# Kernel optimization log

Hardware: AMD Instinct MI355X
Metric: run time of the kernel (lower is better)

Reference implementation:

```python
import jax, jax.numpy as jnp
import numpy as np

B, S, E = 8, 2048, 1024
DROPOUT_P = 0.1


def setup_inputs() -> dict:
    key = jax.random.key(0)
    kq, kk, kv, km, kw, kb = jax.random.split(key, 6)
    query = jax.random.normal(kq, (B, S, E), dtype=jnp.float32)
    key_t = jax.random.normal(kk, (B, S, E), dtype=jnp.float32)
    value = jax.random.normal(kv, (B, S, E), dtype=jnp.float32)
    # inverted dropout mask: keep with prob 1-p, scale kept by 1/(1-p)
    keep = jax.random.bernoulli(km, 1.0 - DROPOUT_P, (B, S, S))
    dropout_mask = keep.astype(jnp.float32) / (1.0 - DROPOUT_P)
    Wout = jax.random.normal(kw, (E, E), dtype=jnp.float32) * (E ** -0.5)
    bout = jax.random.normal(kb, (E,), dtype=jnp.float32) * 0.01
    return {
        "query": query,
        "key": key_t,
        "value": value,
        "dropout_mask": dropout_mask,
        "Wout": Wout,
        "bout": bout,
        "inv_scale_factor": 32,  # sqrt(E) = sqrt(1024)
    }


def reference(query, key, value, dropout_mask, Wout, bout, inv_scale_factor):
    # scores: [B, S, S]
    scores = jnp.einsum("bqd,bkd->bqk", query, key) / jnp.float32(inv_scale_factor)
    probs = jax.nn.softmax(scores, axis=-1)
    probs = probs * dropout_mask  # inverted dropout
    attn = jnp.einsum("bqk,bkd->bqd", probs, value)  # [B, S, E]
    # fc_out: torch Linear -> x @ W.T + b
    return jnp.einsum("bqd,ed->bqe", attn, Wout) + bout
```

## Files before the change

kernel.cpp:

```cpp
#include <hip/hip_runtime.h>
#include <cstdint>
#include <cstddef>

typedef short short8 __attribute__((ext_vector_type(8)));
typedef float f32x4 __attribute__((ext_vector_type(4)));

static __device__ __forceinline__ ushort f2bf(float f) {
  union { float f; uint32_t u; } v; v.f = f;
  uint32_t u = v.u + 0x7fffu + ((v.u >> 16) & 1u);
  return (ushort)(u >> 16);
}
static __device__ __forceinline__ float b2f(uint32_t u) {
  union { uint32_t u; float f; } v; v.u = u << 16;
  return v.f;
}

static __device__ __forceinline__ void g2lds16(const ushort* g, ushort* lds) {
  __builtin_amdgcn_global_load_lds(
      (const __attribute__((address_space(1))) void*)(uintptr_t)g,
      (__attribute__((address_space(3))) void*)(uintptr_t)lds,
      16, 0, 0);
}

__global__ __launch_bounds__(256) void convert_qk_bf16(
    const float* __restrict__ Q, const float* __restrict__ K,
    ushort* __restrict__ Qb, ushort* __restrict__ Kb) {
  const bool second = blockIdx.x >= 8192;
  const float* src = second ? K : Q;
  ushort* dst = second ? Kb : Qb;
  const size_t i = ((size_t)(blockIdx.x & 8191) * 256 + threadIdx.x) * 8;
  const float4 a = *(const float4*)(src + i);
  const float4 b = *(const float4*)(src + i + 4);
  ushort4 o0, o1;
  o0.x = f2bf(a.x); o0.y = f2bf(a.y); o0.z = f2bf(a.z); o0.w = f2bf(a.w);
  o1.x = f2bf(b.x); o1.y = f2bf(b.y); o1.z = f2bf(b.z); o1.w = f2bf(b.w);
  *(ushort4*)(dst + i) = o0;
  *(ushort4*)(dst + i + 4) = o1;
}

__global__ __launch_bounds__(256) void transpose_convert_v(
    const float* __restrict__ V, ushort* __restrict__ Vt) {
  __shared__ float t[32][33];
  const int b = blockIdx.z;
  const int d0 = blockIdx.x * 32;
  const int k0 = blockIdx.y * 32;
  const int tx = threadIdx.x, ty = threadIdx.y;
  const float* Vb = V + (size_t)b * 2048 * 1024;
  ushort* Vtb = Vt + (size_t)b * 1024 * 2048;
#pragma unroll
  for (int j = 0; j < 32; j += 8)
    t[ty + j][tx] = Vb[(size_t)(k0 + ty + j) * 1024 + d0 + tx];
  __syncthreads();
  const int l = ty * 32 + tx;
  const int kk = (l & 15) * 2;
  const int dd = l >> 4;
#pragma unroll
  for (int p = 0; p < 2; ++p) {
    const int d = dd + p * 16;
    const uint32_t val =
        (uint32_t)f2bf(t[kk][d]) | ((uint32_t)f2bf(t[kk + 1][d]) << 16);
    *(uint32_t*)&Vtb[(size_t)(d0 + d) * 2048 + k0 + kk] = val;
  }
}

template <bool B_F32, bool OUT_BF16, bool BIAS>
__global__ __launch_bounds__(256) void gemm_bt(
    const ushort* __restrict__ Ap, const void* __restrict__ Bp,
    void* __restrict__ Cp, int M, int N, int K,
    size_t sA, size_t sB, size_t sC, float scale,
    const float* __restrict__ bias) {
  constexpr int BK = 64;
  constexpr int LDB = B_F32 ? 72 : 64;
  __shared__ __align__(16) ushort As[128 * 64];
  __shared__ __align__(16) ushort Bs[128 * LDB];
  const int tid = threadIdx.x;
  const int z = blockIdx.z;
  const int bm = blockIdx.y, bn = blockIdx.x;
  const int lane = tid & 63, w = tid >> 6;
  const int quad = lane >> 4, l16 = lane & 15;
  const int row0 = (w & 1) * 64, col0 = (w >> 1) * 64;
  const int srow = lane >> 3;
  const int scol = ((lane & 7) ^ srow) * 8;

  f32x4 acc[4][4];
#pragma unroll
  for (int i = 0; i < 4; ++i)
#pragma unroll
    for (int j = 0; j < 4; ++j) acc[i][j] = (f32x4){0.f, 0.f, 0.f, 0.f};

  const ushort* Abase = Ap + sA * z + (size_t)bm * 128 * K;

  for (int k0 = 0; k0 < K; k0 += BK) {
#pragma unroll
    for (int i = 0; i < 4; ++i) {
      const int rbase = w * 8 + i * 32;
      g2lds16(Abase + (size_t)(rbase + srow) * K + k0 + scol, &As[rbase * 64]);
    }
    if constexpr (B_F32) {
      const float* B = (const float*)Bp + sB * z + (size_t)bn * 128 * K + k0;
      int r = tid >> 4;
      const int c = (tid & 15) * 4;
#pragma unroll
      for (int i = 0; i < 8; ++i, r += 16) {
        const float4 v = *(const float4*)(B + (size_t)r * K + c);
        ushort4 o;
        o.x = f2bf(v.x); o.y = f2bf(v.y); o.z = f2bf(v.z); o.w = f2bf(v.w);
        *(ushort4*)&Bs[r * LDB + c] = o;
      }
    } else {
      const ushort* B = (const ushort*)Bp + sB * z + (size_t)bn * 128 * K + k0;
#pragma unroll
      for (int i = 0; i < 4; ++i) {
        const int rbase = w * 8 + i * 32;
        g2lds16(B + (size_t)(rbase + srow) * K + scol, &Bs[rbase * 64]);
      }
    }
    __syncthreads();
#pragma unroll
    for (int kc = 0; kc < BK; kc += 32) {
      const int gidx = (kc >> 3) + quad;
      short8 af[4], bfr[4];
#pragma unroll
      for (int tm = 0; tm < 4; ++tm) {
        const int row = row0 + tm * 16 + l16;
        af[tm] = *(const short8*)&As[row * 64 + ((gidx ^ (row & 7)) << 3)];
      }
#pragma unroll
      for (int tn = 0; tn < 4; ++tn) {
        const int row = col0 + tn * 16 + l16;
        if constexpr (B_F32)
          bfr[tn] = *(const short8*)&Bs[row * LDB + kc + quad * 8];
        else
          bfr[tn] = *(const short8*)&Bs[row * 64 + ((gidx ^ (row & 7)) << 3)];
      }
#pragma unroll
      for (int tm = 0; tm < 4; ++tm)
#pragma unroll
        for (int tn = 0; tn < 4; ++tn)
          acc[tm][tn] = __builtin_amdgcn_mfma_f32_16x16x32_bf16(
              af[tm], bfr[tn], acc[tm][tn], 0, 0, 0);
    }
    __syncthreads();
  }
#pragma unroll
  for (int tn = 0; tn < 4; ++tn) {
    const int gc = bn * 128 + col0 + tn * 16 + l16;
    const float bv = BIAS ? bias[gc] : 0.f;
#pragma unroll
    for (int tm = 0; tm < 4; ++tm) {
      const int grb = bm * 128 + row0 + tm * 16 + quad * 4;
#pragma unroll
      for (int r = 0; r < 4; ++r) {
        const float v = acc[tm][tn][r] * scale + bv;
        const size_t idx = (size_t)(grb + r) * N + gc;
        if constexpr (OUT_BF16)
          ((ushort*)Cp + sC * z)[idx] = f2bf(v);
        else
          ((float*)Cp + sC * z)[idx] = v;
      }
    }
  }
}

__global__ __launch_bounds__(256) void softmax_dropout(
    ushort* __restrict__ P, const float* __restrict__ mask) {
  const int row = blockIdx.x;
  const size_t off = (size_t)row * 2048 + (size_t)threadIdx.x * 8;
  ushort* p = P + off;
  const float* mk = mask + off;
  const uint4 raw = *(const uint4*)p;
  float s[8];
  s[0] = b2f(raw.x & 0xffffu); s[1] = b2f(raw.x >> 16);
  s[2] = b2f(raw.y & 0xffffu); s[3] = b2f(raw.y >> 16);
  s[4] = b2f(raw.z & 0xffffu); s[5] = b2f(raw.z >> 16);
  s[6] = b2f(raw.w & 0xffffu); s[7] = b2f(raw.w >> 16);
  float m = s[0];
#pragma unroll
  for (int i = 1; i < 8; ++i) m = fmaxf(m, s[i]);
#pragma unroll
  for (int o = 32; o >= 1; o >>= 1) m = fmaxf(m, __shfl_xor(m, o));
  __shared__ float redm[4], reds[4];
  const int wv = threadIdx.x >> 6;
  if ((threadIdx.x & 63) == 0) redm[wv] = m;
  __syncthreads();
  m = fmaxf(fmaxf(redm[0], redm[1]), fmaxf(redm[2], redm[3]));
  float e[8], l = 0.f;
#pragma unroll
  for (int i = 0; i < 8; ++i) { e[i] = __expf(s[i] - m); l += e[i]; }
#pragma unroll
  for (int o = 32; o >= 1; o >>= 1) l += __shfl_xor(l, o);
  if ((threadIdx.x & 63) == 0) reds[wv] = l;
  __syncthreads();
  l = (reds[0] + reds[1]) + (reds[2] + reds[3]);
  const float inv = 1.0f / l;
  const float4 m0 = *(const float4*)mk;
  const float4 m1 = *(const float4*)(mk + 4);
  float q[8];
  q[0] = e[0] * inv * m0.x; q[1] = e[1] * inv * m0.y;
  q[2] = e[2] * inv * m0.z; q[3] = e[3] * inv * m0.w;
  q[4] = e[4] * inv * m1.x; q[5] = e[5] * inv * m1.y;
  q[6] = e[6] * inv * m1.z; q[7] = e[7] * inv * m1.w;
  uint4 o;
  o.x = (uint32_t)f2bf(q[0]) | ((uint32_t)f2bf(q[1]) << 16);
  o.y = (uint32_t)f2bf(q[2]) | ((uint32_t)f2bf(q[3]) << 16);
  o.z = (uint32_t)f2bf(q[4]) | ((uint32_t)f2bf(q[5]) << 16);
  o.w = (uint32_t)f2bf(q[6]) | ((uint32_t)f2bf(q[7]) << 16);
  *(uint4*)p = o;
}

extern "C" void kernel_launch(void* const* d_in, const int* in_sizes, int n_in,
                              void* d_out, int out_size, void* d_ws,
                              size_t ws_size, hipStream_t stream) {
  (void)in_sizes; (void)n_in; (void)out_size; (void)ws_size;
  const float* Q    = (const float*)d_in[0];
  const float* Kmat = (const float*)d_in[1];
  const float* V    = (const float*)d_in[2];
  const float* mask = (const float*)d_in[3];
  const float* W    = (const float*)d_in[4];
  const float* bout = (const float*)d_in[5];
  float* out = (float*)d_out;

  ushort* RegA = (ushort*)d_ws;
  ushort* RegB = RegA + (size_t)16 * 1024 * 1024;
  ushort* P    = RegB + (size_t)16 * 1024 * 1024;

  convert_qk_bf16<<<dim3(16384), 256, 0, stream>>>(Q, Kmat, RegA, RegB);
  gemm_bt<false, true, false><<<dim3(16, 16, 8), 256, 0, stream>>>(
      RegA, RegB, P, 2048, 2048, 1024,
      (size_t)2048 * 1024, (size_t)2048 * 1024, (size_t)2048 * 2048,
      1.0f / 32.0f, nullptr);
  transpose_convert_v<<<dim3(32, 64, 8), dim3(32, 8), 0, stream>>>(V, RegA);
  softmax_dropout<<<dim3(16384), 256, 0, stream>>>(P, mask);
  gemm_bt<false, true, false><<<dim3(8, 16, 8), 256, 0, stream>>>(
      P, RegA, RegB, 2048, 1024, 2048,
      (size_t)2048 * 2048, (size_t)1024 * 2048, (size_t)2048 * 1024,
      1.0f, nullptr);
  gemm_bt<true, false, true><<<dim3(8, 128, 1), 256, 0, stream>>>(
      RegB, W, out, 16384, 1024, 1024, 0, 0, 0, 1.0f, bout);
}
```

Before: 613.9 us.

## Replace GEMMs with 256x256-tile, 4-stage async-LDS pipelined kernel; pre-convert W

Replaces the 128x128 single-buffered GEMM with a 256x256 tile kernel using 512 threads, BK=32 and a 4-deep ring of LDS buffers filled by global_load_lds, drained with vmcnt waits plus barriers so loads overlap MFMA compute. It also raises MFMA priority during compute and uses a new XOR swizzle. The output projection's W matrix is now converted to bf16 by a separate kernel instead of inside the GEMM. The aim is to hide global memory latency and raise data reuse per tile. The cost is more LDS and registers per block and fewer blocks for the smaller grids.

```diff
diff --git a/kernel.cpp b/kernel.cpp
--- a/kernel.cpp
+++ b/kernel.cpp
@@ -38,6 +38,18 @@
   *(ushort4*)(dst + i + 4) = o1;
 }
 
+__global__ __launch_bounds__(256) void convert_w_bf16(
+    const float* __restrict__ W, ushort* __restrict__ Wb) {
+  const size_t i = ((size_t)blockIdx.x * 256 + threadIdx.x) * 8;
+  const float4 a = *(const float4*)(W + i);
+  const float4 b = *(const float4*)(W + i + 4);
+  ushort4 o0, o1;
+  o0.x = f2bf(a.x); o0.y = f2bf(a.y); o0.z = f2bf(a.z); o0.w = f2bf(a.w);
+  o1.x = f2bf(b.x); o1.y = f2bf(b.y); o1.z = f2bf(b.z); o1.w = f2bf(b.w);
+  *(ushort4*)(Wb + i) = o0;
+  *(ushort4*)(Wb + i + 4) = o1;
+}
+
 __global__ __launch_bounds__(256) void transpose_convert_v(
     const float* __restrict__ V, ushort* __restrict__ Vt) {
   __shared__ float t[32][33];
@@ -63,100 +75,103 @@
   }
 }
 
-template <bool B_F32, bool OUT_BF16, bool BIAS>
-__global__ __launch_bounds__(256) void gemm_bt(
-    const ushort* __restrict__ Ap, const void* __restrict__ Bp,
+#define DRAIN_BAR(n) asm volatile("s_waitcnt vmcnt(" #n ")\n\ts_barrier" ::: "memory")
+
+template <bool OUT_BF16, bool BIAS>
+__global__ __launch_bounds__(512, 2) void gemm256(
+    const ushort* __restrict__ Ap, const ushort* __restrict__ Bp,
     void* __restrict__ Cp, int M, int N, int K,
     size_t sA, size_t sB, size_t sC, float scale,
     const float* __restrict__ bias) {
-  constexpr int BK = 64;
-  constexpr int LDB = B_F32 ? 72 : 64;
-  __shared__ __align__(16) ushort As[128 * 64];
-  __shared__ __align__(16) ushort Bs[128 * LDB];
+  constexpr int BK = 32;
+  __shared__ __align__(16) ushort As[4][256 * BK];
+  __shared__ __align__(16) ushort Bs[4][256 * BK];
   const int tid = threadIdx.x;
   const int z = blockIdx.z;
   const int bm = blockIdx.y, bn = blockIdx.x;
   const int lane = tid & 63, w = tid >> 6;
   const int quad = lane >> 4, l16 = lane & 15;
-  const int row0 = (w & 1) * 64, col0 = (w >> 1) * 64;
-  const int srow = lane >> 3;
-  const int scol = ((lane & 7) ^ srow) * 8;
-
-  f32x4 acc[4][4];
-#pragma unroll
-  for (int i = 0; i < 4; ++i)
+  const int wm = w >> 2, wn = w & 3;
+  const int NT = K >> 5;
+
+  f32x4 acc[8][4];
+#pragma unroll
+  for (int i = 0; i < 8; ++i)
 #pragma unroll
     for (int j = 0; j < 4; ++j) acc[i][j] = (f32x4){0.f, 0.f, 0.f, 0.f};
 
-  const ushort* Abase = Ap + sA * z + (size_t)bm * 128 * K;
-
-  for (int k0 = 0; k0 < K; k0 += BK) {
-#pragma unroll
-    for (int i = 0; i < 4; ++i) {
-      const int rbase = w * 8 + i * 32;
-      g2lds16(Abase + (size_t)(rbase + srow) * K + k0 + scol, &As[rbase * 64]);
-    }
-    if constexpr (B_F32) {
-      const float* B = (const float*)Bp + sB * z + (size_t)bn * 128 * K + k0;
-      int r = tid >> 4;
-      const int c = (tid & 15) * 4;
-#pragma unroll
-      for (int i = 0; i < 8; ++i, r += 16) {
-        const float4 v = *(const float4*)(B + (size_t)r * K + c);
-        ushort4 o;
-        o.x = f2bf(v.x); o.y = f2bf(v.y); o.z = f2bf(v.z); o.w = f2bf(v.w);
-        *(ushort4*)&Bs[r * LDB + c] = o;
-      }
-    } else {
-      const ushort* B = (const ushort*)Bp + sB * z + (size_t)bn * 128 * K + k0;
-#pragma unroll
-      for (int i = 0; i < 4; ++i) {
-        const int rbase = w * 8 + i * 32;
-        g2lds16(B + (size_t)(rbase + srow) * K + scol, &Bs[rbase * 64]);
-      }
-    }
-    __syncthreads();
-#pragma unroll
-    for (int kc = 0; kc < BK; kc += 32) {
-      const int gidx = (kc >> 3) + quad;
-      short8 af[4], bfr[4];
-#pragma unroll
-      for (int tm = 0; tm < 4; ++tm) {
-        const int row = row0 + tm * 16 + l16;
-        af[tm] = *(const short8*)&As[row * 64 + ((gidx ^ (row & 7)) << 3)];
-      }
-#pragma unroll
-      for (int tn = 0; tn < 4; ++tn) {
-        const int row = col0 + tn * 16 + l16;
-        if constexpr (B_F32)
-          bfr[tn] = *(const short8*)&Bs[row * LDB + kc + quad * 8];
-        else
-          bfr[tn] = *(const short8*)&Bs[row * 64 + ((gidx ^ (row & 7)) << 3)];
-      }
-#pragma unroll
-      for (int tm = 0; tm < 4; ++tm)
-#pragma unroll
-        for (int tn = 0; tn < 4; ++tn)
-          acc[tm][tn] = __builtin_amdgcn_mfma_f32_16x16x32_bf16(
-              af[tm], bfr[tn], acc[tm][tn], 0, 0, 0);
-    }
-    __syncthreads();
+  const int srow = w * 16 + (lane >> 2);
+  const int sgran = (lane & 3) ^ ((lane >> 3) & 3);
+  const ushort* Abase = Ap + sA * z + (size_t)bm * 256 * K;
+  const ushort* Bbase = Bp + sB * z + (size_t)bn * 256 * K;
+  const ushort* Ag0 = Abase + (size_t)srow * K + sgran * 8;
+  const ushort* Ag1 = Ag0 + (size_t)128 * K;
+  const ushort* Bg0 = Bbase + (size_t)srow * K + sgran * 8;
+  const ushort* Bg1 = Bg0 + (size_t)128 * K;
+  const int ldsw0 = (w * 16) * BK;
+  const int ldsw1 = (128 + w * 16) * BK;
+
+  auto STAGE = [&](int t) {
+    ushort* a = As[t & 3];
+    ushort* b = Bs[t & 3];
+    const size_t ko = (size_t)t * BK;
+    g2lds16(Ag0 + ko, a + ldsw0);
+    g2lds16(Ag1 + ko, a + ldsw1);
+    g2lds16(Bg0 + ko, b + ldsw0);
+    g2lds16(Bg1 + ko, b + ldsw1);
+  };
+
+  const int pg = quad ^ ((l16 >> 1) & 3);
+  const int aoff = (wm * 128 + l16) * BK + pg * 8;
+  const int boff = (wn * 64 + l16) * BK + pg * 8;
+
+  auto COMPUTE = [&](int t) {
+    const ushort* a = As[t & 3];
+    const ushort* b = Bs[t & 3];
+    short8 bf[4], af[8];
+#pragma unroll
+    for (int tn = 0; tn < 4; ++tn)
+      bf[tn] = *(const short8*)&b[boff + tn * 16 * BK];
+#pragma unroll
+    for (int tm = 0; tm < 8; ++tm)
+      af[tm] = *(const short8*)&a[aoff + tm * 16 * BK];
+    __builtin_amdgcn_s_setprio(1);
+#pragma unroll
+    for (int tm = 0; tm < 8; ++tm)
+#pragma unroll
+      for (int tn = 0; tn < 4; ++tn)
+        acc[tm][tn] = __builtin_amdgcn_mfma_f32_16x16x32_bf16(
+            af[tm], bf[tn], acc[tm][tn], 0, 0, 0);
+    __builtin_amdgcn_s_setprio(0);
+  };
+
+  STAGE(0); STAGE(1); STAGE(2);
+  for (int t = 0; t < NT - 2; ++t) {
+    DRAIN_BAR(8);
+    if (t + 3 < NT) STAGE(t + 3);
+    COMPUTE(t);
   }
+  DRAIN_BAR(4);
+  COMPUTE(NT - 2);
+  DRAIN_BAR(0);
+  COMPUTE(NT - 1);
+
+  const size_t cz = sC * z;
 #pragma unroll
   for (int tn = 0; tn < 4; ++tn) {
-    const int gc = bn * 128 + col0 + tn * 16 + l16;
+    const int gc = bn * 256 + wn * 64 + tn * 16 + l16;
     const float bv = BIAS ? bias[gc] : 0.f;
 #pragma unroll
-    for (int tm = 0; tm < 4; ++tm) {
-      const int grb = bm * 128 + row0 + tm * 16 + quad * 4;
+    for (int tm = 0; tm < 8; ++tm) {
+      const int grb = bm * 256 + wm * 128 + tm * 16 + quad * 4;
 #pragma unroll
       for (int r = 0; r < 4; ++r) {
         const float v = acc[tm][tn][r] * scale + bv;
         const size_t idx = (size_t)(grb + r) * N + gc;
         if constexpr (OUT_BF16)
-          ((ushort*)Cp + sC * z)[idx] = f2bf(v);
+          ((ushort*)Cp + cz)[idx] = f2bf(v);
         else
-          ((float*)Cp + sC * z)[idx] = v;
+          ((float*)Cp + cz)[idx] = v;
       }
     }
   }
@@ -225,16 +240,17 @@
   ushort* P    = RegB + (size_t)16 * 1024 * 1024;
 
   convert_qk_bf16<<<dim3(16384), 256, 0, stream>>>(Q, Kmat, RegA, RegB);
-  gemm_bt<false, true, false><<<dim3(16, 16, 8), 256, 0, stream>>>(
+  gemm256<true, false><<<dim3(8, 8, 8), 512, 0, stream>>>(
       RegA, RegB, P, 2048, 2048, 1024,
       (size_t)2048 * 1024, (size_t)2048 * 1024, (size_t)2048 * 2048,
       1.0f / 32.0f, nullptr);
   transpose_convert_v<<<dim3(32, 64, 8), dim3(32, 8), 0, stream>>>(V, RegA);
   softmax_dropout<<<dim3(16384), 256, 0, stream>>>(P, mask);
-  gemm_bt<false, true, false><<<dim3(8, 16, 8), 256, 0, stream>>>(
+  gemm256<true, false><<<dim3(4, 8, 8), 512, 0, stream>>>(
       P, RegA, RegB, 2048, 1024, 2048,
       (size_t)2048 * 2048, (size_t)1024 * 2048, (size_t)2048 * 1024,
       1.0f, nullptr);
-  gemm_bt<true, false, true><<<dim3(8, 128, 1), 256, 0, stream>>>(
-      RegB, W, out, 16384, 1024, 1024, 0, 0, 0, 1.0f, bout);
-}
+  convert_w_bf16<<<dim3(512), 256, 0, stream>>>(W, RegA);
+  gemm256<false, true><<<dim3(4, 64, 1), 512, 0, stream>>>(
+      RegB, RegA, out, 16384, 1024, 1024, 0, 0, 0, 1.0f, bout);
+}
```

Result: faster. 547.1 us (-10.9%).
